# Optimization experiments

Measured on AMD Instinct MI355X. Metric: run time of the kernel, lower is better.

Reference implementation:

```python
import jax, jax.numpy as jnp
import numpy as np

C = 343.0                      # wave speed
OMEGA = 2.0 * np.pi * 1000.0   # angular frequency
K2 = (C / OMEGA) ** 2          # coefficient on u in the (as-written) residual

N_POINTS = 262144
HIDDEN = 256


def _mlp_point(p, W1, b1, W2, b2, W3, b3, W4, b4):
    # p: (3,) -> scalar u(x,y,z); tanh MLP stand-in for model_estimation
    h = jnp.tanh(p @ W1 + b1)
    h = jnp.tanh(h @ W2 + b2)
    h = jnp.tanh(h @ W3 + b3)
    return (h @ W4 + b4)[0]


def setup_inputs() -> dict:
    key = jax.random.key(0)
    ks = jax.random.split(key, 5)

    def init_w(k, fan_in, fan_out):
        return jax.random.normal(k, (fan_in, fan_out), dtype=jnp.float32) / np.sqrt(fan_in).astype(np.float32)

    inputs = jax.random.normal(ks[0], (N_POINTS, 3), dtype=jnp.float32)
    W1 = init_w(ks[1], 3, HIDDEN)
    W2 = init_w(ks[2], HIDDEN, HIDDEN)
    W3 = init_w(ks[3], HIDDEN, HIDDEN)
    W4 = init_w(ks[4], HIDDEN, 1)
    z = lambda n: jnp.zeros((n,), dtype=jnp.float32)
    return {
        "inputs": inputs,
        "W1": W1, "b1": z(HIDDEN),
        "W2": W2, "b2": z(HIDDEN),
        "W3": W3, "b3": z(HIDDEN),
        "W4": W4, "b4": z(1),
    }


def reference(inputs, W1, b1, W2, b2, W3, b3, W4, b4):
    # Per-point scalar field u(p); Laplacian = trace of the 3x3 Hessian.
    def u_point(p):
        return _mlp_point(p, W1, b1, W2, b2, W3, b3, W4, b4)

    u = jax.vmap(u_point)(inputs)                       # [N]
    hess = jax.vmap(jax.hessian(u_point))(inputs)       # [N, 3, 3]
    laplace_u = hess[:, 0, 0] + hess[:, 1, 1] + hess[:, 2, 2]  # [N]

    pde_residual = laplace_u + K2 * u
    return jnp.mean(jnp.abs(pde_residual) ** 2)
```

## Files before the change

### kernel.cpp

```cpp
#include <hip/hip_runtime.h>
#include <math.h>

#define HID 256
#define PTS 16
#define NSTR 5
#define ROWS (NSTR*PTS)
#define PITCH 272

typedef __fp16  fp16x2 __attribute__((ext_vector_type(2)));
typedef _Float16 half8  __attribute__((ext_vector_type(8)));
typedef float   floatx4 __attribute__((ext_vector_type(4)));

constexpr double PI_D = 3.14159265358979323846;
constexpr float K2F = (float)((343.0/(2.0*PI_D*1000.0))*(343.0/(2.0*PI_D*1000.0)));

union H2U { fp16x2 h; unsigned int u; };
__device__ __forceinline__ unsigned int pk(float a, float b) {
  H2U t; t.h = __builtin_amdgcn_cvt_pkrtz(a, b); return t.u;
}

__device__ __forceinline__ float tanh_fast(float z) {
  float e = __builtin_amdgcn_exp2f(z * 2.8853900817779268f);
  return 1.0f - 2.0f * __builtin_amdgcn_rcpf(e + 1.0f);
}

__global__ void pack_kernel(const float* __restrict__ W2, const float* __restrict__ W3,
                            _Float16* __restrict__ out) {
  int t = blockIdx.x * blockDim.x + threadIdx.x;
  int l    = t >> 13;
  int rem  = t & 8191;
  int kc   = rem >> 10;
  int nt   = (rem >> 6) & 15;
  int lane = rem & 63;
  const float* W = l ? W3 : W2;
  int k0 = kc*32 + ((lane >> 4) << 3);
  int n  = (nt >> 2)*64 + (lane & 15)*4 + (nt & 3);
  _Float16* o = out + (size_t)t * 8;
  #pragma unroll
  for (int j = 0; j < 8; ++j)
    o[j] = (_Float16)W[(size_t)(k0 + j)*HID + n];
}

__global__ __launch_bounds__(256, 3) void helm_kernel(
    const float* __restrict__ inputs,
    const float* __restrict__ W1, const float* __restrict__ b1,
    const float* __restrict__ b2, const float* __restrict__ b3,
    const float* __restrict__ W4, const float* __restrict__ b4,
    const _Float16* __restrict__ Wpack,
    float* __restrict__ part)
{
  __shared__ __align__(16) _Float16 X[ROWS][PITCH];

  const int tid  = threadIdx.x;
  const int lane = tid & 63;
  const int wave = tid >> 6;
  const int m    = lane & 15;
  const int q    = lane >> 4;

  const int pbase = blockIdx.x * PTS;

  {
    const int p  = tid >> 4;
    const int c0 = (tid & 15) * 16;
    const float x0 = inputs[(size_t)(pbase + p)*3 + 0];
    const float x1 = inputs[(size_t)(pbase + p)*3 + 1];
    const float x2 = inputs[(size_t)(pbase + p)*3 + 2];
    #pragma unroll
    for (int ch = 0; ch < 2; ++ch) {
      float v[NSTR][8];
      #pragma unroll
      for (int jj = 0; jj < 2; ++jj) {
        const int n = c0 + ch*8 + jj*4;
        floatx4 w0 = *(const floatx4*)&W1[0*HID + n];
        floatx4 w1 = *(const floatx4*)&W1[1*HID + n];
        floatx4 w2 = *(const floatx4*)&W1[2*HID + n];
        floatx4 bn = *(const floatx4*)&b1[n];
        #pragma unroll
        for (int e = 0; e < 4; ++e) {
          float z  = fmaf(x2, w2[e], fmaf(x1, w1[e], fmaf(x0, w0[e], bn[e])));
          float a  = tanh_fast(z);
          float dd = 1.0f - a*a;
          float wsq = fmaf(w0[e], w0[e], fmaf(w1[e], w1[e], w2[e]*w2[e]));
          v[0][jj*4+e] = a;
          v[1][jj*4+e] = dd*w0[e];
          v[2][jj*4+e] = dd*w1[e];
          v[3][jj*4+e] = dd*w2[e];
          v[4][jj*4+e] = -2.0f*a*dd*wsq;
        }
      }
      #pragma unroll
      for (int s = 0; s < NSTR; ++s) {
        uint4 u;
        u.x = pk(v[s][0], v[s][1]); u.y = pk(v[s][2], v[s][3]);
        u.z = pk(v[s][4], v[s][5]); u.w = pk(v[s][6], v[s][7]);
        *(uint4*)&X[s*PTS + p][c0 + ch*8] = u;
      }
    }
  }
  __syncthreads();

  const int colbase = wave*64 + m*4;

  auto kloop = [&](const _Float16* __restrict__ Wp, floatx4 (&acc)[NSTR][4]) {
    const _Float16* wb = Wp + (((size_t)(wave*4)*64 + lane) << 3);
    #pragma unroll
    for (int kc = 0; kc < 8; ++kc) {
      half8 bfrag[4];
      #pragma unroll
      for (int c = 0; c < 4; ++c)
        bfrag[c] = *(const half8*)(wb + (size_t)kc*8192 + c*512);
      half8 afrag[NSTR];
      #pragma unroll
      for (int s = 0; s < NSTR; ++s)
        afrag[s] = *(const half8*)(&X[s*PTS + m][kc*32 + q*8]);
      #pragma unroll
      for (int s = 0; s < NSTR; ++s)
        #pragma unroll
        for (int c = 0; c < 4; ++c)
          acc[s][c] = __builtin_amdgcn_mfma_f32_16x16x32_f16(afrag[s], bfrag[c], acc[s][c], 0, 0, 0);
    }
  };

  {
    floatx4 acc[NSTR][4];
    #pragma unroll
    for (int s = 0; s < NSTR; ++s)
      #pragma unroll
      for (int c = 0; c < 4; ++c)
        acc[s][c] = (floatx4){0.0f, 0.0f, 0.0f, 0.0f};
    kloop(Wpack, acc);
    __syncthreads();

    floatx4 bv = *(const floatx4*)&b2[colbase];
    #pragma unroll
    for (int r = 0; r < 4; ++r) {
      const int p = q*4 + r;
      float va[4], vg0[4], vg1[4], vg2[4], vT[4];
      #pragma unroll
      for (int c = 0; c < 4; ++c) {
        float z  = acc[0][c][r] + bv[c];
        float a  = tanh_fast(z);
        float dd = 1.0f - a*a;
        float z0 = acc[1][c][r], z1 = acc[2][c][r], z2 = acc[3][c][r];
        float zpp = acc[4][c][r];
        float s2 = fmaf(z0, z0, fmaf(z1, z1, z2*z2));
        va[c]  = a;
        vg0[c] = dd*z0; vg1[c] = dd*z1; vg2[c] = dd*z2;
        vT[c]  = fmaf(dd, zpp, -2.0f*a*dd*s2);
      }
      uint2 u;
      u.x = pk(va[0],va[1]);   u.y = pk(va[2],va[3]);   *(uint2*)&X[0*PTS + p][colbase] = u;
      u.x = pk(vg0[0],vg0[1]); u.y = pk(vg0[2],vg0[3]); *(uint2*)&X[1*PTS + p][colbase] = u;
      u.x = pk(vg1[0],vg1[1]); u.y = pk(vg1[2],vg1[3]); *(uint2*)&X[2*PTS + p][colbase] = u;
      u.x = pk(vg2[0],vg2[1]); u.y = pk(vg2[2],vg2[3]); *(uint2*)&X[3*PTS + p][colbase] = u;
      u.x = pk(vT[0],vT[1]);   u.y = pk(vT[2],vT[3]);   *(uint2*)&X[4*PTS + p][colbase] = u;
    }
    __syncthreads();
  }

  {
    floatx4 acc[NSTR][4];
    #pragma unroll
    for (int s = 0; s < NSTR; ++s)
      #pragma unroll
      for (int c = 0; c < 4; ++c)
        acc[s][c] = (floatx4){0.0f, 0.0f, 0.0f, 0.0f};
    kloop(Wpack + 65536, acc);
    __syncthreads();

    floatx4 bv = *(const floatx4*)&b3[colbase];
    floatx4 w4 = *(const floatx4*)&W4[colbase];
    float su[4] = {0,0,0,0}, st[4] = {0,0,0,0};
    #pragma unroll
    for (int r = 0; r < 4; ++r)
      #pragma unroll
      for (int c = 0; c < 4; ++c) {
        float z  = acc[0][c][r] + bv[c];
        float a  = tanh_fast(z);
        float dd = 1.0f - a*a;
        float z0 = acc[1][c][r], z1 = acc[2][c][r], z2 = acc[3][c][r];
        float zpp = acc[4][c][r];
        float s2 = fmaf(z0, z0, fmaf(z1, z1, z2*z2));
        float T  = fmaf(dd, zpp, -2.0f*a*dd*s2);
        su[r] = fmaf(a, w4[c], su[r]);
        st[r] = fmaf(T, w4[c], st[r]);
      }

    #pragma unroll
    for (int off = 8; off >= 1; off >>= 1)
      #pragma unroll
      for (int r = 0; r < 4; ++r) {
        su[r] += __shfl_down(su[r], off);
        st[r] += __shfl_down(st[r], off);
      }
    float* S = (float*)X;
    if (m == 0) {
      #pragma unroll
      for (int r = 0; r < 4; ++r) {
        S[(q*4 + r)*8 + wave]     = su[r];
        S[(q*4 + r)*8 + 4 + wave] = st[r];
      }
    }
  }
  __syncthreads();

  if (wave == 0) {
    const float* S = (const float*)X;
    int pidx = lane >> 2, w = lane & 3;
    float suc = S[pidx*8 + w];
    float stc = S[pidx*8 + 4 + w];
    suc += __shfl_down(suc, 1); suc += __shfl_down(suc, 2);
    stc += __shfl_down(stc, 1); stc += __shfl_down(stc, 2);
    float sq = 0.0f;
    if ((lane & 3) == 0) {
      float u   = suc + b4[0];
      float res = fmaf(K2F, u, stc);
      sq = res * res;
    }
    sq += __shfl_down(sq, 4); sq += __shfl_down(sq, 8);
    sq += __shfl_down(sq, 16); sq += __shfl_down(sq, 32);
    if (lane == 0) part[blockIdx.x] = sq;
  }
}

__global__ void reduce_kernel(const float* __restrict__ part, float* __restrict__ out,
                              int nblk, float scale) {
  float s = 0.0f;
  for (int i = threadIdx.x; i < (nblk >> 2); i += 256) {
    floatx4 v = *(const floatx4*)&part[i << 2];
    s += (v[0] + v[1]) + (v[2] + v[3]);
  }
  #pragma unroll
  for (int off = 32; off; off >>= 1) s += __shfl_down(s, off);
  __shared__ float sm[4];
  if ((threadIdx.x & 63) == 0) sm[threadIdx.x >> 6] = s;
  __syncthreads();
  if (threadIdx.x == 0) out[0] = ((sm[0] + sm[1]) + (sm[2] + sm[3])) * scale;
}

extern "C" void kernel_launch(void* const* d_in, const int* in_sizes, int n_in,
                              void* d_out, int out_size, void* d_ws, size_t ws_size,
                              hipStream_t stream) {
  const float* inputs = (const float*)d_in[0];
  const float* W1 = (const float*)d_in[1];
  const float* b1 = (const float*)d_in[2];
  const float* W2 = (const float*)d_in[3];
  const float* b2 = (const float*)d_in[4];
  const float* W3 = (const float*)d_in[5];
  const float* b3 = (const float*)d_in[6];
  const float* W4 = (const float*)d_in[7];
  const float* b4 = (const float*)d_in[8];
  float* out = (float*)d_out;

  _Float16* wp   = (_Float16*)d_ws;
  float*    part = (float*)((char*)d_ws + 2*65536*2);

  int N    = in_sizes[0] / 3;
  int nblk = N / PTS;

  pack_kernel<<<64, 256, 0, stream>>>(W2, W3, wp);
  helm_kernel<<<nblk, 256, 0, stream>>>(inputs, W1, b1, b2, b3, W4, b4, wp, part);
  reduce_kernel<<<1, 256, 0, stream>>>(part, out, nblk, 1.0f / (float)N);
}
```

Measured before the change: 408.3 us.

## Ping-pong two point tiles per block to overlap MFMA with tanh epilogues

Each block now handles two 16-point tiles held in two LDS buffers. While the MFMA k-loop runs on one tile, the layer-1 and activation epilogue work for the other tile is interleaved around it, so matrix and vector ALU work can overlap. The padded LDS pitch is replaced by an XOR swizzle to avoid bank conflicts, and s_setprio is raised around the MFMA bursts. The cost is 80KB of dynamic LDS and launch bounds lowered to 2 blocks per CU, which means fewer resident waves and more register pressure from two accumulator sets.

```diff
diff --git a/kernel.cpp b/kernel.cpp
--- a/kernel.cpp
+++ b/kernel.cpp
@@ -5,7 +5,9 @@
 #define PTS 16
 #define NSTR 5
 #define ROWS (NSTR*PTS)
-#define PITCH 272
+#define TBUF 20480
+
+#define XI(r,c) ((((r)<<8) + (c)) ^ (((r)&7)<<3))
 
 typedef __fp16  fp16x2 __attribute__((ext_vector_type(2)));
 typedef _Float16 half8  __attribute__((ext_vector_type(8)));
@@ -41,7 +43,7 @@
     o[j] = (_Float16)W[(size_t)(k0 + j)*HID + n];
 }
 
-__global__ __launch_bounds__(256, 3) void helm_kernel(
+__global__ __launch_bounds__(256, 2) void helm_kernel(
     const float* __restrict__ inputs,
     const float* __restrict__ W1, const float* __restrict__ b1,
     const float* __restrict__ b2, const float* __restrict__ b3,
@@ -49,59 +51,61 @@
     const _Float16* __restrict__ Wpack,
     float* __restrict__ part)
 {
-  __shared__ __align__(16) _Float16 X[ROWS][PITCH];
+  extern __shared__ __align__(16) _Float16 Xs[];
+  _Float16* const XA = Xs;
+  _Float16* const XB = Xs + TBUF;
 
   const int tid  = threadIdx.x;
   const int lane = tid & 63;
   const int wave = tid >> 6;
   const int m    = lane & 15;
   const int q    = lane >> 4;
-
-  const int pbase = blockIdx.x * PTS;
-
-  {
+  const int pbase = blockIdx.x * (2*PTS);
+  const int colbase = wave*64 + m*4;
+
+  auto l1_half = [&](_Float16* __restrict__ Xb, int toff, int ch) {
     const int p  = tid >> 4;
     const int c0 = (tid & 15) * 16;
-    const float x0 = inputs[(size_t)(pbase + p)*3 + 0];
-    const float x1 = inputs[(size_t)(pbase + p)*3 + 1];
-    const float x2 = inputs[(size_t)(pbase + p)*3 + 2];
-    #pragma unroll
-    for (int ch = 0; ch < 2; ++ch) {
-      float v[NSTR][8];
-      #pragma unroll
-      for (int jj = 0; jj < 2; ++jj) {
-        const int n = c0 + ch*8 + jj*4;
-        floatx4 w0 = *(const floatx4*)&W1[0*HID + n];
-        floatx4 w1 = *(const floatx4*)&W1[1*HID + n];
-        floatx4 w2 = *(const floatx4*)&W1[2*HID + n];
-        floatx4 bn = *(const floatx4*)&b1[n];
-        #pragma unroll
-        for (int e = 0; e < 4; ++e) {
-          float z  = fmaf(x2, w2[e], fmaf(x1, w1[e], fmaf(x0, w0[e], bn[e])));
-          float a  = tanh_fast(z);
-          float dd = 1.0f - a*a;
-          float wsq = fmaf(w0[e], w0[e], fmaf(w1[e], w1[e], w2[e]*w2[e]));
-          v[0][jj*4+e] = a;
-          v[1][jj*4+e] = dd*w0[e];
-          v[2][jj*4+e] = dd*w1[e];
-          v[3][jj*4+e] = dd*w2[e];
-          v[4][jj*4+e] = -2.0f*a*dd*wsq;
-        }
-      }
-      #pragma unroll
-      for (int s = 0; s < NSTR; ++s) {
-        uint4 u;
-        u.x = pk(v[s][0], v[s][1]); u.y = pk(v[s][2], v[s][3]);
-        u.z = pk(v[s][4], v[s][5]); u.w = pk(v[s][6], v[s][7]);
-        *(uint4*)&X[s*PTS + p][c0 + ch*8] = u;
-      }
-    }
-  }
-  __syncthreads();
-
-  const int colbase = wave*64 + m*4;
-
-  auto kloop = [&](const _Float16* __restrict__ Wp, floatx4 (&acc)[NSTR][4]) {
+    const float x0 = inputs[(size_t)(pbase + toff + p)*3 + 0];
+    const float x1 = inputs[(size_t)(pbase + toff + p)*3 + 1];
+    const float x2 = inputs[(size_t)(pbase + toff + p)*3 + 2];
+    float v[NSTR][8];
+    #pragma unroll
+    for (int jj = 0; jj < 2; ++jj) {
+      const int n = c0 + ch*8 + jj*4;
+      floatx4 w0 = *(const floatx4*)&W1[0*HID + n];
+      floatx4 w1 = *(const floatx4*)&W1[1*HID + n];
+      floatx4 w2 = *(const floatx4*)&W1[2*HID + n];
+      floatx4 bn = *(const floatx4*)&b1[n];
+      #pragma unroll
+      for (int e = 0; e < 4; ++e) {
+        float z  = fmaf(x2, w2[e], fmaf(x1, w1[e], fmaf(x0, w0[e], bn[e])));
+        float a  = tanh_fast(z);
+        float dd = 1.0f - a*a;
+        float wsq = fmaf(w0[e], w0[e], fmaf(w1[e], w1[e], w2[e]*w2[e]));
+        v[0][jj*4+e] = a;
+        v[1][jj*4+e] = dd*w0[e];
+        v[2][jj*4+e] = dd*w1[e];
+        v[3][jj*4+e] = dd*w2[e];
+        v[4][jj*4+e] = -2.0f*a*dd*wsq;
+      }
+    }
+    #pragma unroll
+    for (int s = 0; s < NSTR; ++s) {
+      uint4 u;
+      u.x = pk(v[s][0], v[s][1]); u.y = pk(v[s][2], v[s][3]);
+      u.z = pk(v[s][4], v[s][5]); u.w = pk(v[s][6], v[s][7]);
+      *(uint4*)&Xb[XI(s*PTS + p, c0 + ch*8)] = u;
+    }
+  };
+
+  auto kloop = [&](const _Float16* __restrict__ Wp, const _Float16* __restrict__ Xb,
+                   floatx4 (&acc)[NSTR][4]) {
+    #pragma unroll
+    for (int s = 0; s < NSTR; ++s)
+      #pragma unroll
+      for (int c = 0; c < 4; ++c)
+        acc[s][c] = (floatx4){0.0f, 0.0f, 0.0f, 0.0f};
     const _Float16* wb = Wp + (((size_t)(wave*4)*64 + lane) << 3);
     #pragma unroll
     for (int kc = 0; kc < 8; ++kc) {
@@ -112,80 +116,68 @@
       half8 afrag[NSTR];
       #pragma unroll
       for (int s = 0; s < NSTR; ++s)
-        afrag[s] = *(const half8*)(&X[s*PTS + m][kc*32 + q*8]);
+        afrag[s] = *(const half8*)(&Xb[XI(s*PTS + m, kc*32 + q*8)]);
+      __builtin_amdgcn_s_setprio(1);
       #pragma unroll
       for (int s = 0; s < NSTR; ++s)
         #pragma unroll
         for (int c = 0; c < 4; ++c)
           acc[s][c] = __builtin_amdgcn_mfma_f32_16x16x32_f16(afrag[s], bfrag[c], acc[s][c], 0, 0, 0);
-    }
-  };
-
-  {
-    floatx4 acc[NSTR][4];
-    #pragma unroll
-    for (int s = 0; s < NSTR; ++s)
-      #pragma unroll
-      for (int c = 0; c < 4; ++c)
-        acc[s][c] = (floatx4){0.0f, 0.0f, 0.0f, 0.0f};
-    kloop(Wpack, acc);
-    __syncthreads();
-
-    floatx4 bv = *(const floatx4*)&b2[colbase];
+      __builtin_amdgcn_s_setprio(0);
+    }
+  };
+
+  auto c2_half = [&](_Float16* __restrict__ Xb, const float* __restrict__ bb,
+                     floatx4 (&acc)[NSTR][4], int h) {
+    const float bv0 = bb[colbase + 2*h + 0];
+    const float bv1 = bb[colbase + 2*h + 1];
     #pragma unroll
     for (int r = 0; r < 4; ++r) {
       const int p = q*4 + r;
-      float va[4], vg0[4], vg1[4], vg2[4], vT[4];
-      #pragma unroll
-      for (int c = 0; c < 4; ++c) {
-        float z  = acc[0][c][r] + bv[c];
+      float o0[NSTR], o1[NSTR];
+      #pragma unroll
+      for (int c2 = 0; c2 < 2; ++c2) {
+        const int c = 2*h + c2;
+        float z  = acc[0][c][r] + (c2 ? bv1 : bv0);
         float a  = tanh_fast(z);
         float dd = 1.0f - a*a;
         float z0 = acc[1][c][r], z1 = acc[2][c][r], z2 = acc[3][c][r];
         float zpp = acc[4][c][r];
         float s2 = fmaf(z0, z0, fmaf(z1, z1, z2*z2));
-        va[c]  = a;
-        vg0[c] = dd*z0; vg1[c] = dd*z1; vg2[c] = dd*z2;
-        vT[c]  = fmaf(dd, zpp, -2.0f*a*dd*s2);
-      }
-      uint2 u;
-      u.x = pk(va[0],va[1]);   u.y = pk(va[2],va[3]);   *(uint2*)&X[0*PTS + p][colbase] = u;
-      u.x = pk(vg0[0],vg0[1]); u.y = pk(vg0[2],vg0[3]); *(uint2*)&X[1*PTS + p][colbase] = u;
-      u.x = pk(vg1[0],vg1[1]); u.y = pk(vg1[2],vg1[3]); *(uint2*)&X[2*PTS + p][colbase] = u;
-      u.x = pk(vg2[0],vg2[1]); u.y = pk(vg2[2],vg2[3]); *(uint2*)&X[3*PTS + p][colbase] = u;
-      u.x = pk(vT[0],vT[1]);   u.y = pk(vT[2],vT[3]);   *(uint2*)&X[4*PTS + p][colbase] = u;
-    }
-    __syncthreads();
-  }
-
-  {
-    floatx4 acc[NSTR][4];
-    #pragma unroll
-    for (int s = 0; s < NSTR; ++s)
-      #pragma unroll
-      for (int c = 0; c < 4; ++c)
-        acc[s][c] = (floatx4){0.0f, 0.0f, 0.0f, 0.0f};
-    kloop(Wpack + 65536, acc);
-    __syncthreads();
-
-    floatx4 bv = *(const floatx4*)&b3[colbase];
-    floatx4 w4 = *(const floatx4*)&W4[colbase];
-    float su[4] = {0,0,0,0}, st[4] = {0,0,0,0};
-    #pragma unroll
-    for (int r = 0; r < 4; ++r)
-      #pragma unroll
-      for (int c = 0; c < 4; ++c) {
-        float z  = acc[0][c][r] + bv[c];
+        float* o = c2 ? o1 : o0;
+        o[0] = a;
+        o[1] = dd*z0; o[2] = dd*z1; o[3] = dd*z2;
+        o[4] = fmaf(dd, zpp, -2.0f*a*dd*s2);
+      }
+      #pragma unroll
+      for (int s = 0; s < NSTR; ++s)
+        *(unsigned int*)&Xb[XI(s*PTS + p, colbase + 2*h)] = pk(o0[s], o1[s]);
+    }
+  };
+
+  auto e3_half = [&](floatx4 (&acc)[NSTR][4], int h,
+                     float (&su)[4], float (&st)[4]) {
+    #pragma unroll
+    for (int c2 = 0; c2 < 2; ++c2) {
+      const int c = 2*h + c2;
+      const float bv  = b3[colbase + c];
+      const float w4v = W4[colbase + c];
+      #pragma unroll
+      for (int r = 0; r < 4; ++r) {
+        float z  = acc[0][c][r] + bv;
         float a  = tanh_fast(z);
         float dd = 1.0f - a*a;
         float z0 = acc[1][c][r], z1 = acc[2][c][r], z2 = acc[3][c][r];
         float zpp = acc[4][c][r];
         float s2 = fmaf(z0, z0, fmaf(z1, z1, z2*z2));
         float T  = fmaf(dd, zpp, -2.0f*a*dd*s2);
-        su[r] = fmaf(a, w4[c], su[r]);
-        st[r] = fmaf(T, w4[c], st[r]);
-      }
-
+        su[r] = fmaf(a, w4v, su[r]);
+        st[r] = fmaf(T, w4v, st[r]);
+      }
+    }
+  };
+
+  auto epilogue = [&](float (&su)[4], float (&st)[4], int t) {
     #pragma unroll
     for (int off = 8; off >= 1; off >>= 1)
       #pragma unroll
@@ -193,7 +185,7 @@
         su[r] += __shfl_down(su[r], off);
         st[r] += __shfl_down(st[r], off);
       }
-    float* S = (float*)X;
+    float* S = (float*)Xs + t*128;
     if (m == 0) {
       #pragma unroll
       for (int r = 0; r < 4; ++r) {
@@ -201,21 +193,57 @@
         S[(q*4 + r)*8 + 4 + wave] = st[r];
       }
     }
-  }
+  };
+
+  floatx4 accA[NSTR][4], accB[NSTR][4];
+  float suA[4] = {0,0,0,0}, stA[4] = {0,0,0,0};
+  float suB[4] = {0,0,0,0}, stB[4] = {0,0,0,0};
+
+  l1_half(XA, 0, 0);
+  l1_half(XA, 0, 1);
+  __syncthreads();
+
+  l1_half(XB, PTS, 0);
+  kloop(Wpack, XA, accA);
+  l1_half(XB, PTS, 1);
+  __syncthreads();
+
+  c2_half(XA, b2, accA, 0);
+  kloop(Wpack, XB, accB);
+  c2_half(XA, b2, accA, 1);
+  __syncthreads();
+
+  c2_half(XB, b2, accB, 0);
+  kloop(Wpack + 65536, XA, accA);
+  c2_half(XB, b2, accB, 1);
+  __syncthreads();
+
+  e3_half(accA, 0, suA, stA);
+  kloop(Wpack + 65536, XB, accB);
+  e3_half(accA, 1, suA, stA);
+  epilogue(suA, stA, 0);
+  __syncthreads();
+
+  e3_half(accB, 0, suB, stB);
+  e3_half(accB, 1, suB, stB);
+  epilogue(suB, stB, 1);
   __syncthreads();
 
   if (wave == 0) {
-    const float* S = (const float*)X;
+    const float* S = (const float*)Xs;
     int pidx = lane >> 2, w = lane & 3;
-    float suc = S[pidx*8 + w];
-    float stc = S[pidx*8 + 4 + w];
-    suc += __shfl_down(suc, 1); suc += __shfl_down(suc, 2);
-    stc += __shfl_down(stc, 1); stc += __shfl_down(stc, 2);
     float sq = 0.0f;
-    if ((lane & 3) == 0) {
-      float u   = suc + b4[0];
-      float res = fmaf(K2F, u, stc);
-      sq = res * res;
+    #pragma unroll
+    for (int t = 0; t < 2; ++t) {
+      float suc = S[t*128 + pidx*8 + w];
+      float stc = S[t*128 + pidx*8 + 4 + w];
+      suc += __shfl_down(suc, 1); suc += __shfl_down(suc, 2);
+      stc += __shfl_down(stc, 1); stc += __shfl_down(stc, 2);
+      if ((lane & 3) == 0) {
+        float u   = suc + b4[0];
+        float res = fmaf(K2F, u, stc);
+        sq += res * res;
+      }
     }
     sq += __shfl_down(sq, 4); sq += __shfl_down(sq, 8);
     sq += __shfl_down(sq, 16); sq += __shfl_down(sq, 32);
@@ -255,10 +283,17 @@
   _Float16* wp   = (_Float16*)d_ws;
   float*    part = (float*)((char*)d_ws + 2*65536*2);
 
+  static int attr_done = 0;
+  if (!attr_done) {
+    hipFuncSetAttribute(reinterpret_cast<const void*>(helm_kernel),
+                        hipFuncAttributeMaxDynamicSharedMemorySize, 2*TBUF*2);
+    attr_done = 1;
+  }
+
   int N    = in_sizes[0] / 3;
-  int nblk = N / PTS;
+  int nblk = N / (2*PTS);
 
   pack_kernel<<<64, 256, 0, stream>>>(W2, W3, wp);
-  helm_kernel<<<nblk, 256, 0, stream>>>(inputs, W1, b1, b2, b3, W4, b4, wp, part);
+  helm_kernel<<<nblk, 256, 2*TBUF*2, stream>>>(inputs, W1, b1, b2, b3, W4, b4, wp, part);
   reduce_kernel<<<1, 256, 0, stream>>>(part, out, nblk, 1.0f / (float)N);
 }
```

After: 459.2 us. +12.4%, slower.

## Swizzle LDS activations, software-pipeline MFMA fragment loads, precompute W1 norms

Applied to the files above, without the earlier changes.

XORs the LDS column index by row parity to change the bank mapping of the activation tile. Restructures the k-loop so the next chunk's global weight fragments and the next stream's LDS A-fragment are loaded while the current MFMAs issue. Moves the per-column squared norm of W1 into an extra block of the pack kernel so the main kernel reads it instead of recomputing it. These aim to hide load latency and cut LDS bank conflicts, at the cost of more live registers under the 3-block occupancy bound.

```diff
diff --git a/kernel.cpp b/kernel.cpp
--- a/kernel.cpp
+++ b/kernel.cpp
@@ -6,6 +6,7 @@
 #define NSTR 5
 #define ROWS (NSTR*PTS)
 #define PITCH 272
+#define XS(r,c) ((c) ^ (((r)&1)<<3))
 
 typedef __fp16  fp16x2 __attribute__((ext_vector_type(2)));
 typedef _Float16 half8  __attribute__((ext_vector_type(8)));
@@ -25,7 +26,14 @@
 }
 
 __global__ void pack_kernel(const float* __restrict__ W2, const float* __restrict__ W3,
-                            _Float16* __restrict__ out) {
+                            const float* __restrict__ W1,
+                            _Float16* __restrict__ out, float* __restrict__ wsq) {
+  if (blockIdx.x == 64) {
+    int n = threadIdx.x;
+    float w0 = W1[0*HID + n], w1 = W1[1*HID + n], w2 = W1[2*HID + n];
+    wsq[n] = fmaf(w0, w0, fmaf(w1, w1, w2*w2));
+    return;
+  }
   int t = blockIdx.x * blockDim.x + threadIdx.x;
   int l    = t >> 13;
   int rem  = t & 8191;
@@ -47,6 +55,7 @@
     const float* __restrict__ b2, const float* __restrict__ b3,
     const float* __restrict__ W4, const float* __restrict__ b4,
     const _Float16* __restrict__ Wpack,
+    const float* __restrict__ wsqv,
     float* __restrict__ part)
 {
   __shared__ __align__(16) _Float16 X[ROWS][PITCH];
@@ -75,17 +84,17 @@
         floatx4 w1 = *(const floatx4*)&W1[1*HID + n];
         floatx4 w2 = *(const floatx4*)&W1[2*HID + n];
         floatx4 bn = *(const floatx4*)&b1[n];
+        floatx4 ws = *(const floatx4*)&wsqv[n];
         #pragma unroll
         for (int e = 0; e < 4; ++e) {
           float z  = fmaf(x2, w2[e], fmaf(x1, w1[e], fmaf(x0, w0[e], bn[e])));
           float a  = tanh_fast(z);
           float dd = 1.0f - a*a;
-          float wsq = fmaf(w0[e], w0[e], fmaf(w1[e], w1[e], w2[e]*w2[e]));
           v[0][jj*4+e] = a;
           v[1][jj*4+e] = dd*w0[e];
           v[2][jj*4+e] = dd*w1[e];
           v[3][jj*4+e] = dd*w2[e];
-          v[4][jj*4+e] = -2.0f*a*dd*wsq;
+          v[4][jj*4+e] = -2.0f*a*dd*ws[e];
         }
       }
       #pragma unroll
@@ -93,7 +102,7 @@
         uint4 u;
         u.x = pk(v[s][0], v[s][1]); u.y = pk(v[s][2], v[s][3]);
         u.z = pk(v[s][4], v[s][5]); u.w = pk(v[s][6], v[s][7]);
-        *(uint4*)&X[s*PTS + p][c0 + ch*8] = u;
+        *(uint4*)&X[s*PTS + p][XS(p, c0 + ch*8)] = u;
       }
     }
   }
@@ -103,21 +112,31 @@
 
   auto kloop = [&](const _Float16* __restrict__ Wp, floatx4 (&acc)[NSTR][4]) {
     const _Float16* wb = Wp + (((size_t)(wave*4)*64 + lane) << 3);
+    half8 bnxt[4];
+    #pragma unroll
+    for (int c = 0; c < 4; ++c)
+      bnxt[c] = *(const half8*)(wb + c*512);
     #pragma unroll
     for (int kc = 0; kc < 8; ++kc) {
-      half8 bfrag[4];
-      #pragma unroll
-      for (int c = 0; c < 4; ++c)
-        bfrag[c] = *(const half8*)(wb + (size_t)kc*8192 + c*512);
-      half8 afrag[NSTR];
-      #pragma unroll
-      for (int s = 0; s < NSTR; ++s)
-        afrag[s] = *(const half8*)(&X[s*PTS + m][kc*32 + q*8]);
-      #pragma unroll
-      for (int s = 0; s < NSTR; ++s)
+      half8 bcur[4];
+      #pragma unroll
+      for (int c = 0; c < 4; ++c) bcur[c] = bnxt[c];
+      if (kc < 7) {
         #pragma unroll
         for (int c = 0; c < 4; ++c)
-          acc[s][c] = __builtin_amdgcn_mfma_f32_16x16x32_f16(afrag[s], bfrag[c], acc[s][c], 0, 0, 0);
+          bnxt[c] = *(const half8*)(wb + (size_t)(kc+1)*8192 + c*512);
+      }
+      half8 acur = *(const half8*)(&X[0*PTS + m][XS(m, kc*32 + q*8)]);
+      #pragma unroll
+      for (int s = 0; s < NSTR; ++s) {
+        half8 anxt;
+        if (s + 1 < NSTR)
+          anxt = *(const half8*)(&X[(s+1)*PTS + m][XS(m, kc*32 + q*8)]);
+        #pragma unroll
+        for (int c = 0; c < 4; ++c)
+          acc[s][c] = __builtin_amdgcn_mfma_f32_16x16x32_f16(acur, bcur[c], acc[s][c], 0, 0, 0);
+        if (s + 1 < NSTR) acur = anxt;
+      }
     }
   };
 
@@ -148,12 +167,13 @@
         vg0[c] = dd*z0; vg1[c] = dd*z1; vg2[c] = dd*z2;
         vT[c]  = fmaf(dd, zpp, -2.0f*a*dd*s2);
       }
+      const int cs = XS(p, colbase);
       uint2 u;
-      u.x = pk(va[0],va[1]);   u.y = pk(va[2],va[3]);   *(uint2*)&X[0*PTS + p][colbase] = u;
-      u.x = pk(vg0[0],vg0[1]); u.y = pk(vg0[2],vg0[3]); *(uint2*)&X[1*PTS + p][colbase] = u;
-      u.x = pk(vg1[0],vg1[1]); u.y = pk(vg1[2],vg1[3]); *(uint2*)&X[2*PTS + p][colbase] = u;
-      u.x = pk(vg2[0],vg2[1]); u.y = pk(vg2[2],vg2[3]); *(uint2*)&X[3*PTS + p][colbase] = u;
-      u.x = pk(vT[0],vT[1]);   u.y = pk(vT[2],vT[3]);   *(uint2*)&X[4*PTS + p][colbase] = u;
+      u.x = pk(va[0],va[1]);   u.y = pk(va[2],va[3]);   *(uint2*)&X[0*PTS + p][cs] = u;
+      u.x = pk(vg0[0],vg0[1]); u.y = pk(vg0[2],vg0[3]); *(uint2*)&X[1*PTS + p][cs] = u;
+      u.x = pk(vg1[0],vg1[1]); u.y = pk(vg1[2],vg1[3]); *(uint2*)&X[2*PTS + p][cs] = u;
+      u.x = pk(vg2[0],vg2[1]); u.y = pk(vg2[2],vg2[3]); *(uint2*)&X[3*PTS + p][cs] = u;
+      u.x = pk(vT[0],vT[1]);   u.y = pk(vT[2],vT[3]);   *(uint2*)&X[4*PTS + p][cs] = u;
     }
     __syncthreads();
   }
@@ -254,11 +274,12 @@
 
   _Float16* wp   = (_Float16*)d_ws;
   float*    part = (float*)((char*)d_ws + 2*65536*2);
+  float*    wsq  = (float*)((char*)d_ws + 2*65536*2 + 65536);
 
   int N    = in_sizes[0] / 3;
   int nblk = N / PTS;
 
-  pack_kernel<<<64, 256, 0, stream>>>(W2, W3, wp);
-  helm_kernel<<<nblk, 256, 0, stream>>>(inputs, W1, b1, b2, b3, W4, b4, wp, part);
+  pack_kernel<<<65, 256, 0, stream>>>(W2, W3, W1, wp, wsq);
+  helm_kernel<<<nblk, 256, 0, stream>>>(inputs, W1, b1, b2, b3, W4, b4, wp, wsq, part);
   reduce_kernel<<<1, 256, 0, stream>>>(part, out, nblk, 1.0f / (float)N);
 }
```

After: 433.4 us. +6.1%, slower.
